# Optimization experiments

Hardware: AMD Instinct MI355X
Metric: run time of the kernel (lower is better)

Reference implementation:

```python
import jax, jax.numpy as jnp
import numpy as np

B, SQ, SKV, D = 4, 4096, 4096, 64

def setup_inputs() -> dict:
    key = jax.random.key(0)
    kq, kv = jax.random.split(key)
    query = jax.random.normal(kq, (B, SQ, D), dtype=jnp.float32)
    value = jax.random.normal(kv, (B, SKV, D), dtype=jnp.float32)
    return {"query": query, "value": value}

def reference(query, value):
    # scores = Q @ V^T  (value acts as both keys and values; no 1/sqrt(d) scaling)
    scores = jnp.einsum('bqd,bkd->bqk', query, value)  # [B, SQ, SKV]
    dist = jax.nn.softmax(scores, axis=-1)
    context = jnp.einsum('bqk,bkd->bqd', dist, value)  # [B, SQ, D]
    return context
```

## Files before the change

### kernel.cpp

```cpp
#include <hip/hip_runtime.h>


#define NB   4
#define SQ   4096
#define SKV  4096
#define DH   64
#define L2E  1.44269504088896340736f

typedef _Float16 half8 __attribute__((ext_vector_type(8)));
typedef _Float16 half4 __attribute__((ext_vector_type(4)));
typedef _Float16 half2v __attribute__((ext_vector_type(2)));
typedef float f32x4 __attribute__((ext_vector_type(4)));
typedef unsigned short u16;

#define MFMA16(a, b, c) __builtin_amdgcn_mfma_f32_16x16x16f16((a), (b), (c), 0, 0, 0)
#define MFMA32(a, b, c) __builtin_amdgcn_mfma_f32_16x16x32_f16((a), (b), (c), 0, 0, 0)

__device__ __forceinline__ u16 f2h(float f) {
  _Float16 h = (_Float16)f;
  return __builtin_bit_cast(u16, h);
}
__device__ __forceinline__ half2v pkrtz(float a, float b) {
  return __builtin_bit_cast(half2v, __builtin_amdgcn_cvt_pkrtz(a, b));
}

__global__ __launch_bounds__(256) void prep_kernel(
    const float* __restrict__ V, u16* __restrict__ vh, u16* __restrict__ vt) {
  __shared__ u16 ldsT[16 * 72];
  int blk = blockIdx.x;
  int b   = blk >> 8;
  int rem = blk & 255;
  int j0  = (rem >> 2) << 6;
  int d0  = (rem & 3) << 4;
  int t   = threadIdx.x;
  int j   = t >> 2;
  int dc  = (t & 3) << 2;

  const float* src = V + ((size_t)(b * SKV) + j0 + j) * DH + d0 + dc;
  float4 v4 = *(const float4*)src;
  u16 h[4] = {f2h(v4.x), f2h(v4.y), f2h(v4.z), f2h(v4.w)};
  unsigned p0 = (unsigned)h[0] | ((unsigned)h[1] << 16);
  unsigned p1 = (unsigned)h[2] | ((unsigned)h[3] << 16);
  size_t go = ((size_t)(b * SKV) + j0 + j) * DH + d0 + dc;
  *(uint2*)(vh + go) = make_uint2(p0, p1);

#pragma unroll
  for (int k = 0; k < 4; ++k) ldsT[(dc + k) * 72 + j] = h[k];
  __syncthreads();

  int dl = t >> 4;
  int jc = (t & 15) << 2;
  u16 tr[4];
#pragma unroll
  for (int k = 0; k < 4; ++k) tr[k] = ldsT[dl * 72 + jc + k];
  unsigned q0 = (unsigned)tr[0] | ((unsigned)tr[1] << 16);
  unsigned q1 = (unsigned)tr[2] | ((unsigned)tr[3] << 16);
  *(uint2*)(vt + ((size_t)(b * DH) + d0 + dl) * SKV + j0 + jc) = make_uint2(q0, q1);
}

__global__ __launch_bounds__(256, 4) void attn_kernel(
    const float* __restrict__ Q,
    const u16* __restrict__ vh,
    const u16* __restrict__ vt,
    u16* __restrict__ po,
    float* __restrict__ pm,
    float* __restrict__ pl,
    int S, int kvLen) {
  __shared__ __align__(16) u16 lds[2][2][64 * 72];

  int blk  = blockIdx.x;
  int tile = blk / S;
  int s    = blk - tile * S;
  int b    = tile >> 5;
  int q0   = (tile & 31) << 7;
  int kv0  = s * kvLen;
  int t    = threadIdx.x;
  int wave = t >> 6;
  int lane = t & 63;
  int col  = lane & 15;
  int quad = lane >> 4;
  int qw   = q0 + (wave << 5);

  half8 qf[2][2];
#pragma unroll
  for (int set = 0; set < 2; ++set) {
#pragma unroll
    for (int kc = 0; kc < 2; ++kc) {
      const float* qp = Q + ((size_t)(b * SQ) + qw + set * 16 + col) * DH +
                        kc * 32 + (quad << 3);
      float4 a0 = *(const float4*)qp;
      float4 a1 = *(const float4*)(qp + 4);
      half8 h;
      h[0] = (_Float16)(a0.x * L2E); h[1] = (_Float16)(a0.y * L2E);
      h[2] = (_Float16)(a0.z * L2E); h[3] = (_Float16)(a0.w * L2E);
      h[4] = (_Float16)(a1.x * L2E); h[5] = (_Float16)(a1.y * L2E);
      h[6] = (_Float16)(a1.z * L2E); h[7] = (_Float16)(a1.w * L2E);
      qf[set][kc] = h;
    }
  }

  f32x4 o[2][4];
  float m_r[2] = {-1e30f, -1e30f};
  float l_r[2] = {0.f, 0.f};
#pragma unroll
  for (int set = 0; set < 2; ++set)
#pragma unroll
    for (int nf = 0; nf < 4; ++nf) o[set][nf] = (f32x4){0.f, 0.f, 0.f, 0.f};

  int sr = t >> 2;
  int sc = (t & 3) << 4;
  const u16* gv  = vh + (size_t)(b * SKV) * DH;
  const u16* gvt = vt + (size_t)(b * DH) * SKV;
  int l0 = sr * 72 + sc;

  {
    size_t g  = (size_t)(kv0 + sr) * DH + sc;
    size_t gt = (size_t)sr * SKV + kv0 + sc;
    *(uint4*)(&lds[0][0][l0])     = *(const uint4*)(gv + g);
    *(uint4*)(&lds[0][0][l0 + 8]) = *(const uint4*)(gv + g + 8);
    *(uint4*)(&lds[0][1][l0])     = *(const uint4*)(gvt + gt);
    *(uint4*)(&lds[0][1][l0 + 8]) = *(const uint4*)(gvt + gt + 8);
  }

  int nIter = kvLen >> 6;
  int cur = 0;
  for (int it = 0; it < nIter; ++it) {
    __syncthreads();

    const u16* sv  = &lds[cur][0][0];
    const u16* svt = &lds[cur][1][0];

    f32x4 sf[2][4];
#pragma unroll
    for (int set = 0; set < 2; ++set)
#pragma unroll
      for (int nf = 0; nf < 4; ++nf) sf[set][nf] = (f32x4){0.f, 0.f, 0.f, 0.f};
#pragma unroll
    for (int nf = 0; nf < 4; ++nf) {
#pragma unroll
      for (int kc = 0; kc < 2; ++kc) {
        half8 av = *(const half8*)(sv + (nf * 16 + col) * 72 + kc * 32 + (quad << 3));
        sf[0][nf] = MFMA32(av, qf[0][kc], sf[0][nf]);
        sf[1][nf] = MFMA32(av, qf[1][kc], sf[1][nf]);
      }
    }

    half4 pf[2][4];
#pragma unroll
    for (int set = 0; set < 2; ++set) {
      float tm = sf[set][0][0];
#pragma unroll
      for (int nf = 0; nf < 4; ++nf)
#pragma unroll
        for (int r = 0; r < 4; ++r) tm = fmaxf(tm, sf[set][nf][r]);
      tm = fmaxf(tm, __shfl_xor(tm, 16, 64));
      tm = fmaxf(tm, __shfl_xor(tm, 32, 64));
      float mn = fmaxf(m_r[set], tm);
      float al = exp2f(m_r[set] - mn);
      m_r[set] = mn;
      float rs = 0.f;
#pragma unroll
      for (int nf = 0; nf < 4; ++nf) {
        float p0 = exp2f(sf[set][nf][0] - mn);
        float p1 = exp2f(sf[set][nf][1] - mn);
        float p2 = exp2f(sf[set][nf][2] - mn);
        float p3 = exp2f(sf[set][nf][3] - mn);
        rs += (p0 + p1) + (p2 + p3);
        half2v lo = pkrtz(p0, p1);
        half2v hi = pkrtz(p2, p3);
        pf[set][nf] = __builtin_shufflevector(lo, hi, 0, 1, 2, 3);
      }
      l_r[set] = l_r[set] * al + rs;
#pragma unroll
      for (int nf = 0; nf < 4; ++nf)
#pragma unroll
        for (int r = 0; r < 4; ++r) o[set][nf][r] *= al;
    }

#pragma unroll
    for (int kc4 = 0; kc4 < 4; ++kc4) {
#pragma unroll
      for (int nf2 = 0; nf2 < 4; ++nf2) {
        half4 avt = *(const half4*)(svt + (nf2 * 16 + col) * 72 + kc4 * 16 + (quad << 2));
        o[0][nf2] = MFMA16(avt, pf[0][kc4], o[0][nf2]);
        o[1][nf2] = MFMA16(avt, pf[1][kc4], o[1][nf2]);
      }
    }

    if ((it + 1) < nIter) {
      int j0n = kv0 + ((it + 1) << 6);
      size_t g  = (size_t)(j0n + sr) * DH + sc;
      size_t gt = (size_t)sr * SKV + j0n + sc;
      uint4 a0 = *(const uint4*)(gv + g);
      uint4 a1 = *(const uint4*)(gv + g + 8);
      uint4 c0 = *(const uint4*)(gvt + gt);
      uint4 c1 = *(const uint4*)(gvt + gt + 8);
      u16* dv  = &lds[cur ^ 1][0][0];
      u16* dvt = &lds[cur ^ 1][1][0];
      *(uint4*)(dv + l0)      = a0;
      *(uint4*)(dv + l0 + 8)  = a1;
      *(uint4*)(dvt + l0)     = c0;
      *(uint4*)(dvt + l0 + 8) = c1;
    }
    cur ^= 1;
  }

#pragma unroll
  for (int set = 0; set < 2; ++set) {
    l_r[set] += __shfl_xor(l_r[set], 16, 64);
    l_r[set] += __shfl_xor(l_r[set], 32, 64);
  }
  int pidx = tile * S + s;
  if (quad == 0) {
#pragma unroll
    for (int set = 0; set < 2; ++set) {
      int row = (wave << 5) + set * 16 + col;
      pm[(size_t)pidx * 128 + row] = m_r[set];
      pl[(size_t)pidx * 128 + row] = l_r[set];
    }
  }

  __syncthreads();
  u16* tp = &lds[0][0][0];
#pragma unroll
  for (int set = 0; set < 2; ++set) {
    int q = (wave << 5) + set * 16 + col;
#pragma unroll
    for (int nf2 = 0; nf2 < 4; ++nf2) {
#pragma unroll
      for (int r2 = 0; r2 < 4; r2 += 2) {
        unsigned pk = (unsigned)f2h(o[set][nf2][r2]) |
                      ((unsigned)f2h(o[set][nf2][r2 + 1]) << 16);
        int d = nf2 * 16 + (quad << 2) + r2;
        *(unsigned*)(tp + q * 72 + d) = pk;
      }
    }
  }
  __syncthreads();
  {
    u16* pob = po + (size_t)pidx * 128 * 64;
    int q = t >> 1, hc = (t & 1) << 5;
    uint4 x0 = *(const uint4*)(tp + q * 72 + hc);
    uint4 x1 = *(const uint4*)(tp + q * 72 + hc + 8);
    uint4 x2 = *(const uint4*)(tp + q * 72 + hc + 16);
    uint4 x3 = *(const uint4*)(tp + q * 72 + hc + 24);
    *(uint4*)(pob + q * 64 + hc)      = x0;
    *(uint4*)(pob + q * 64 + hc + 8)  = x1;
    *(uint4*)(pob + q * 64 + hc + 16) = x2;
    *(uint4*)(pob + q * 64 + hc + 24) = x3;
  }
}

__global__ __launch_bounds__(256) void combine_kernel(
    const u16* __restrict__ po,
    const float* __restrict__ pm,
    const float* __restrict__ pl,
    float* __restrict__ out, int S) {
  int t    = threadIdx.x;
  int rowg = blockIdx.x * 32 + (t >> 3);
  int tile = rowg >> 7;
  int row  = rowg & 127;
  int dc   = (t & 7) << 3;

  float mv[8], lv[8];
  float M = -1e30f;
  for (int s = 0; s < S; ++s) {
    mv[s] = pm[(size_t)(tile * S + s) * 128 + row];
    lv[s] = pl[(size_t)(tile * S + s) * 128 + row];
    M = fmaxf(M, mv[s]);
  }
  float L = 0.f, w[8];
  for (int s = 0; s < S; ++s) {
    w[s] = exp2f(mv[s] - M);
    L += lv[s] * w[s];
  }
  float acc[8] = {0.f, 0.f, 0.f, 0.f, 0.f, 0.f, 0.f, 0.f};
  for (int s = 0; s < S; ++s) {
    const u16* p = po + (size_t)(tile * S + s) * 8192 + row * 64 + dc;
    uint4 raw = *(const uint4*)p;
    half8 x = __builtin_bit_cast(half8, raw);
#pragma unroll
    for (int k = 0; k < 8; ++k) acc[k] += w[s] * (float)x[k];
  }
  float invL = 1.0f / L;
  float* op = out + (size_t)rowg * 64 + dc;
  f32x4 o0 = (f32x4){acc[0], acc[1], acc[2], acc[3]};
  f32x4 o1 = (f32x4){acc[4], acc[5], acc[6], acc[7]};
  *(f32x4*)op       = o0 * invL;
  *(f32x4*)(op + 4) = o1 * invL;
}

extern "C" void kernel_launch(void* const* d_in, const int* in_sizes, int n_in,
                              void* d_out, int out_size, void* d_ws, size_t ws_size,
                              hipStream_t stream) {
  const float* Q = (const float*)d_in[0];
  const float* V = (const float*)d_in[1];
  float* out = (float*)d_out;

  const size_t convBytes = (size_t)2 * NB * SKV * DH * 2;
  auto partBytes = [](int S) {
    return (size_t)NB * 32 * S * ((size_t)128 * 64 * 2 + 128 * 8);
  };
  int S = 8;
  while (S > 1 && ws_size < convBytes + partBytes(S)) S >>= 1;
  int kvLen = SKV / S;

  u16* vh = (u16*)d_ws;
  u16* vt = vh + (size_t)NB * SKV * DH;
  u16* po = vt + (size_t)NB * SKV * DH;
  float* pm = (float*)(po + (size_t)NB * 32 * S * 128 * 64);
  float* pl = pm + (size_t)NB * 32 * S * 128;

  prep_kernel<<<NB * 256, 256, 0, stream>>>(V, vh, vt);
  attn_kernel<<<NB * 32 * S, 256, 0, stream>>>(Q, vh, vt, po, pm, pl, S, kvLen);
  combine_kernel<<<NB * SQ / 32, 256, 0, stream>>>(po, pm, pl, out, S);
}
```

Baseline: 111.9 us.

## Stream V tiles into LDS via direct global-to-LDS DMA with XOR swizzle

Replaces the register-staged global-to-LDS copies of the V and V^T tiles with global_load_lds direct transfers, issued at the top of each iteration so they overlap the current tile's MFMA work. Since direct LDS loads cannot pad rows, the padded 72-stride layout becomes a dense 64-stride layout with an XOR chunk swizzle, applied in global memory by the prep kernel and undone in the LDS read addressing. Occupancy hint drops from 4 to 3 blocks per CU. Risks include incorrect swizzle or DMA lane-to-address mapping, and the extra synchronisation needed to be sure the async LDS writes have finished before the next tile is read.

```diff
diff --git a/kernel.cpp b/kernel.cpp
--- a/kernel.cpp
+++ b/kernel.cpp
@@ -22,6 +22,12 @@
 }
 __device__ __forceinline__ half2v pkrtz(float a, float b) {
   return __builtin_bit_cast(half2v, __builtin_amdgcn_cvt_pkrtz(a, b));
+}
+
+typedef __attribute__((address_space(1))) void gvoid;
+typedef __attribute__((address_space(3))) void lvoid;
+__device__ __forceinline__ void dma16(const u16* g, u16* l) {
+  __builtin_amdgcn_global_load_lds((gvoid*)g, (lvoid*)l, 16, 0, 0);
 }
 
 __global__ __launch_bounds__(256) void prep_kernel(
@@ -41,8 +47,9 @@
   u16 h[4] = {f2h(v4.x), f2h(v4.y), f2h(v4.z), f2h(v4.w)};
   unsigned p0 = (unsigned)h[0] | ((unsigned)h[1] << 16);
   unsigned p1 = (unsigned)h[2] | ((unsigned)h[3] << 16);
-  size_t go = ((size_t)(b * SKV) + j0 + j) * DH + d0 + dc;
-  *(uint2*)(vh + go) = make_uint2(p0, p1);
+  int dfull = d0 + dc;
+  int physd = ((((dfull >> 3) ^ (j & 7)) << 3)) + (dfull & 7);
+  *(uint2*)(vh + ((size_t)(b * SKV) + j0 + j) * DH + physd) = make_uint2(p0, p1);
 
 #pragma unroll
   for (int k = 0; k < 4; ++k) ldsT[(dc + k) * 72 + j] = h[k];
@@ -55,10 +62,12 @@
   for (int k = 0; k < 4; ++k) tr[k] = ldsT[dl * 72 + jc + k];
   unsigned q0 = (unsigned)tr[0] | ((unsigned)tr[1] << 16);
   unsigned q1 = (unsigned)tr[2] | ((unsigned)tr[3] << 16);
-  *(uint2*)(vt + ((size_t)(b * DH) + d0 + dl) * SKV + j0 + jc) = make_uint2(q0, q1);
-}
-
-__global__ __launch_bounds__(256, 4) void attn_kernel(
+  int drow = d0 + dl;
+  int physj = ((((jc >> 3) ^ (drow & 7)) << 3)) + (jc & 7);
+  *(uint2*)(vt + ((size_t)(b * DH) + drow) * SKV + j0 + physj) = make_uint2(q0, q1);
+}
+
+__global__ __launch_bounds__(256, 3) void attn_kernel(
     const float* __restrict__ Q,
     const u16* __restrict__ vh,
     const u16* __restrict__ vt,
@@ -66,7 +75,7 @@
     float* __restrict__ pm,
     float* __restrict__ pl,
     int S, int kvLen) {
-  __shared__ __align__(16) u16 lds[2][2][64 * 72];
+  __shared__ __align__(16) u16 lds[2][2][64 * 64];
 
   int blk  = blockIdx.x;
   int tile = blk / S;
@@ -80,6 +89,14 @@
   int col  = lane & 15;
   int quad = lane >> 4;
   int qw   = q0 + (wave << 5);
+  int c7   = col & 7;
+
+  const u16* gv  = vh + (size_t)(b * SKV) * DH;
+  const u16* gvt = vt + (size_t)(b * DH) * SKV;
+
+  int r0 = t >> 3;
+  int c0 = (t & 7) << 3;
+  int wb = wave << 9;
 
   half8 qf[2][2];
 #pragma unroll
@@ -107,19 +124,13 @@
 #pragma unroll
     for (int nf = 0; nf < 4; ++nf) o[set][nf] = (f32x4){0.f, 0.f, 0.f, 0.f};
 
-  int sr = t >> 2;
-  int sc = (t & 3) << 4;
-  const u16* gv  = vh + (size_t)(b * SKV) * DH;
-  const u16* gvt = vt + (size_t)(b * DH) * SKV;
-  int l0 = sr * 72 + sc;
-
   {
-    size_t g  = (size_t)(kv0 + sr) * DH + sc;
-    size_t gt = (size_t)sr * SKV + kv0 + sc;
-    *(uint4*)(&lds[0][0][l0])     = *(const uint4*)(gv + g);
-    *(uint4*)(&lds[0][0][l0 + 8]) = *(const uint4*)(gv + g + 8);
-    *(uint4*)(&lds[0][1][l0])     = *(const uint4*)(gvt + gt);
-    *(uint4*)(&lds[0][1][l0 + 8]) = *(const uint4*)(gvt + gt + 8);
+    u16* dv  = (u16*)&lds[0][0][0];
+    u16* dvt = (u16*)&lds[0][1][0];
+    dma16(gv + ((size_t)(kv0 + r0) << 6) + c0,        dv + wb);
+    dma16(gv + ((size_t)(kv0 + r0 + 32) << 6) + c0,   dv + 2048 + wb);
+    dma16(gvt + (size_t)r0 * SKV + kv0 + c0,          dvt + wb);
+    dma16(gvt + (size_t)(r0 + 32) * SKV + kv0 + c0,   dvt + 2048 + wb);
   }
 
   int nIter = kvLen >> 6;
@@ -127,6 +138,16 @@
   for (int it = 0; it < nIter; ++it) {
     __syncthreads();
 
+    if ((it + 1) < nIter) {
+      int j0n = kv0 + ((it + 1) << 6);
+      u16* dv  = (u16*)&lds[cur ^ 1][0][0];
+      u16* dvt = (u16*)&lds[cur ^ 1][1][0];
+      dma16(gv + ((size_t)(j0n + r0) << 6) + c0,       dv + wb);
+      dma16(gv + ((size_t)(j0n + r0 + 32) << 6) + c0,  dv + 2048 + wb);
+      dma16(gvt + (size_t)r0 * SKV + j0n + c0,         dvt + wb);
+      dma16(gvt + (size_t)(r0 + 32) * SKV + j0n + c0,  dvt + 2048 + wb);
+    }
+
     const u16* sv  = &lds[cur][0][0];
     const u16* svt = &lds[cur][1][0];
 
@@ -139,7 +160,8 @@
     for (int nf = 0; nf < 4; ++nf) {
 #pragma unroll
       for (int kc = 0; kc < 2; ++kc) {
-        half8 av = *(const half8*)(sv + (nf * 16 + col) * 72 + kc * 32 + (quad << 3));
+        int ch = ((kc << 2) + quad) ^ c7;
+        half8 av = *(const half8*)(sv + ((nf * 16 + col) << 6) + (ch << 3));
         sf[0][nf] = MFMA32(av, qf[0][kc], sf[0][nf]);
         sf[1][nf] = MFMA32(av, qf[1][kc], sf[1][nf]);
       }
@@ -181,27 +203,14 @@
     for (int kc4 = 0; kc4 < 4; ++kc4) {
 #pragma unroll
       for (int nf2 = 0; nf2 < 4; ++nf2) {
-        half4 avt = *(const half4*)(svt + (nf2 * 16 + col) * 72 + kc4 * 16 + (quad << 2));
+        int ch = ((kc4 << 1) + (quad >> 1)) ^ c7;
+        half4 avt = *(const half4*)(svt + ((nf2 * 16 + col) << 6) +
+                                    (ch << 3) + ((quad & 1) << 2));
         o[0][nf2] = MFMA16(avt, pf[0][kc4], o[0][nf2]);
         o[1][nf2] = MFMA16(avt, pf[1][kc4], o[1][nf2]);
       }
     }
 
-    if ((it + 1) < nIter) {
-      int j0n = kv0 + ((it + 1) << 6);
-      size_t g  = (size_t)(j0n + sr) * DH + sc;
-      size_t gt = (size_t)sr * SKV + j0n + sc;
-      uint4 a0 = *(const uint4*)(gv + g);
-      uint4 a1 = *(const uint4*)(gv + g + 8);
-      uint4 c0 = *(const uint4*)(gvt + gt);
-      uint4 c1 = *(const uint4*)(gvt + gt + 8);
-      u16* dv  = &lds[cur ^ 1][0][0];
-      u16* dvt = &lds[cur ^ 1][1][0];
-      *(uint4*)(dv + l0)      = a0;
-      *(uint4*)(dv + l0 + 8)  = a1;
-      *(uint4*)(dvt + l0)     = c0;
-      *(uint4*)(dvt + l0 + 8) = c1;
-    }
     cur ^= 1;
   }
 
@@ -221,7 +230,7 @@
   }
 
   __syncthreads();
-  u16* tp = &lds[0][0][0];
+  u16* tp = (u16*)&lds[0][0][0];
 #pragma unroll
   for (int set = 0; set < 2; ++set) {
     int q = (wave << 5) + set * 16 + col;
```

Result: faster. 109.3 us (-2.3%).
